# Performance work log

Measured on AMD Instinct MI355X. Metric: run time of the kernel, lower is better.

## Reference

```python
import jax, jax.numpy as jnp
import numpy as np

DIM = 768
HEADS = 12
HEAD_DIM = DIM // HEADS
MLP_DIM = 4 * DIM
EPS = 1e-5


def setup_inputs() -> dict:
    key = jax.random.key(0)
    ks = jax.random.split(key, 8)
    s = lambda fan_in: 1.0 / np.sqrt(fan_in)
    return {
        "x": jax.random.normal(ks[0], (2, 2048, DIM), dtype=jnp.float32),
        "ln1_w": jnp.ones((DIM,), jnp.float32),
        "ln1_b": jnp.zeros((DIM,), jnp.float32),
        # weights stored [in, out]
        "qkv_w": jax.random.normal(ks[1], (DIM, 3 * DIM), jnp.float32) * s(DIM),
        "qkv_b": jnp.zeros((3 * DIM,), jnp.float32),
        "proj_w": jax.random.normal(ks[2], (DIM, DIM), jnp.float32) * s(DIM),
        "proj_b": jnp.zeros((DIM,), jnp.float32),
        "ln2_w": jnp.ones((DIM,), jnp.float32),
        "ln2_b": jnp.zeros((DIM,), jnp.float32),
        "lin1_w": jax.random.normal(ks[3], (DIM, MLP_DIM), jnp.float32) * s(DIM),
        "lin1_b": jnp.zeros((MLP_DIM,), jnp.float32),
        "lin2_w": jax.random.normal(ks[4], (MLP_DIM, DIM), jnp.float32) * s(MLP_DIM),
        "lin2_b": jnp.zeros((DIM,), jnp.float32),
    }


def _layernorm(x, w, b):
    mu = jnp.mean(x, axis=-1, keepdims=True)
    var = jnp.mean(jnp.square(x - mu), axis=-1, keepdims=True)
    return (x - mu) * jax.lax.rsqrt(var + EPS) * w + b


def _attention(x, qkv_w, qkv_b, proj_w, proj_b):
    B, N, C = x.shape
    qkv = (x @ qkv_w + qkv_b).reshape(B, N, 3, HEADS, HEAD_DIM)
    q, k, v = qkv[:, :, 0], qkv[:, :, 1], qkv[:, :, 2]  # [B, N, H, Dh]
    scale = HEAD_DIM ** -0.5
    attn = jnp.einsum("bqhd,bkhd->bhqk", q, k) * scale  # full NxN scores
    attn = jax.nn.softmax(attn, axis=-1)
    out = jnp.einsum("bhqk,bkhd->bqhd", attn, v).reshape(B, N, C)
    return out @ proj_w + proj_b


def reference(x, ln1_w, ln1_b, qkv_w, qkv_b, proj_w, proj_b,
              ln2_w, ln2_b, lin1_w, lin1_b, lin2_w, lin2_b):
    x = x + _attention(_layernorm(x, ln1_w, ln1_b), qkv_w, qkv_b, proj_w, proj_b)
    h = _layernorm(x, ln2_w, ln2_b)
    h = jax.nn.gelu(h @ lin1_w + lin1_b, approximate=False) @ lin2_w + lin2_b
    return x + h
```

## Files before the change

### kernel.cpp

```cpp
#include <hip/hip_runtime.h>
#include <math.h>

#define DIM 768
#define NTOK 4096
#define SEQ 2048
#define HEADS 12
#define HD 64

using bf16x8 = __attribute__((ext_vector_type(8))) __bf16;
using f32x4  = __attribute__((ext_vector_type(4))) float;
typedef unsigned short u16;

__device__ inline u16 f2bf(float f) {
  union { float f; unsigned u; } v; v.f = f;
  unsigned r = v.u + 0x7fffu + ((v.u >> 16) & 1u);
  return (u16)(r >> 16);
}

__device__ inline void gl_lds16(const u16* g, u16* l) {
  __builtin_amdgcn_global_load_lds(
      (const __attribute__((address_space(1))) unsigned int*)g,
      (__attribute__((address_space(3))) unsigned int*)l, 16, 0, 0);
}

__global__ __launch_bounds__(256) void ln_kernel(const float* __restrict__ x,
                                                 const float* __restrict__ w,
                                                 const float* __restrict__ b,
                                                 u16* __restrict__ y) {
  int row = blockIdx.x;
  int t = threadIdx.x;
  const float* xr = x + (size_t)row * DIM;
  float v0 = xr[t], v1 = xr[t + 256], v2 = xr[t + 512];
  float s = v0 + v1 + v2;
  float q = v0 * v0 + v1 * v1 + v2 * v2;
  for (int o = 32; o > 0; o >>= 1) {
    s += __shfl_down(s, o, 64);
    q += __shfl_down(q, o, 64);
  }
  __shared__ float ws_[4], wq_[4], mb[2];
  int wid = t >> 6;
  if ((t & 63) == 0) { ws_[wid] = s; wq_[wid] = q; }
  __syncthreads();
  if (t == 0) {
    float S = ws_[0] + ws_[1] + ws_[2] + ws_[3];
    float Q = wq_[0] + wq_[1] + wq_[2] + wq_[3];
    float mean = S * (1.0f / DIM);
    float var = Q * (1.0f / DIM) - mean * mean;
    mb[0] = mean;
    mb[1] = rsqrtf(var + 1e-5f);
  }
  __syncthreads();
  float mean = mb[0], rstd = mb[1];
  u16* yr = y + (size_t)row * DIM;
  yr[t]       = f2bf((v0 - mean) * rstd * w[t]       + b[t]);
  yr[t + 256] = f2bf((v1 - mean) * rstd * w[t + 256] + b[t + 256]);
  yr[t + 512] = f2bf((v2 - mean) * rstd * w[t + 512] + b[t + 512]);
}

__global__ __launch_bounds__(256) void redln_kernel(
    const float* __restrict__ P0, const float* __restrict__ P1,
    const float* __restrict__ bias, const float* __restrict__ res,
    float* __restrict__ x2, const float* __restrict__ lnw,
    const float* __restrict__ lnb, u16* __restrict__ y) {
  int row = blockIdx.x;
  int t = threadIdx.x;
  size_t off = (size_t)row * DIM;
  float v[3];
#pragma unroll
  for (int k = 0; k < 3; ++k) {
    int c = t + k * 256;
    v[k] = P0[off + c] + P1[off + c] + bias[c] + res[off + c];
    x2[off + c] = v[k];
  }
  float s = v[0] + v[1] + v[2];
  float q = v[0] * v[0] + v[1] * v[1] + v[2] * v[2];
  for (int o = 32; o > 0; o >>= 1) {
    s += __shfl_down(s, o, 64);
    q += __shfl_down(q, o, 64);
  }
  __shared__ float ws_[4], wq_[4], mb[2];
  int wid = t >> 6;
  if ((t & 63) == 0) { ws_[wid] = s; wq_[wid] = q; }
  __syncthreads();
  if (t == 0) {
    float S = ws_[0] + ws_[1] + ws_[2] + ws_[3];
    float Q = wq_[0] + wq_[1] + wq_[2] + wq_[3];
    float mean = S * (1.0f / DIM);
    float var = Q * (1.0f / DIM) - mean * mean;
    mb[0] = mean;
    mb[1] = rsqrtf(var + 1e-5f);
  }
  __syncthreads();
  float mean = mb[0], rstd = mb[1];
#pragma unroll
  for (int k = 0; k < 3; ++k) {
    int c = t + k * 256;
    y[off + c] = f2bf((v[k] - mean) * rstd * lnw[c] + lnb[c]);
  }
}

__global__ __launch_bounds__(256) void wcvt_all(
    const float* __restrict__ W0, const float* __restrict__ W1,
    const float* __restrict__ W2, const float* __restrict__ W3,
    u16* __restrict__ T0, u16* __restrict__ T1,
    u16* __restrict__ T2, u16* __restrict__ T3) {
  int id = blockIdx.x;
  const float* W; u16* Wt; int K, N, local;
  if (id < 1728)      { W = W0; Wt = T0; K = 768;  N = 2304; local = id; }
  else if (id < 2304) { W = W1; Wt = T1; K = 768;  N = 768;  local = id - 1728; }
  else if (id < 4608) { W = W2; Wt = T2; K = 768;  N = 3072; local = id - 2304; }
  else                { W = W3; Wt = T3; K = 3072; N = 768;  local = id - 4608; }
  int ntiles = N / 32;
  int n0 = (local % ntiles) * 32, k0 = (local / ntiles) * 32;
  __shared__ float tile[32][33];
  int tid = threadIdx.x;
  int c = tid & 31, r8 = tid >> 5;
#pragma unroll
  for (int p = 0; p < 4; ++p) {
    int k = r8 + p * 8;
    tile[k][c] = W[(size_t)(k0 + k) * N + n0 + c];
  }
  __syncthreads();
#pragma unroll
  for (int p = 0; p < 4; ++p) {
    int n = r8 + p * 8;
    Wt[(size_t)(n0 + n) * K + k0 + c] = f2bf(tile[c][n]);
  }
}

__global__ __launch_bounds__(256) void vtr_kernel(const u16* __restrict__ qkvB,
                                                  u16* __restrict__ vT) {
  __shared__ u16 tile[32][33];
  int v0 = blockIdx.x * 32, j0 = blockIdx.y * 32, b = blockIdx.z;
  int tid = threadIdx.x;
  int c = tid & 31, r8 = tid >> 5;
#pragma unroll
  for (int p = 0; p < 4; ++p) {
    int r = r8 + p * 8;
    tile[r][c] = qkvB[((size_t)(b * SEQ + j0 + r)) * 2304 + 1536 + v0 + c];
  }
  __syncthreads();
#pragma unroll
  for (int p = 0; p < 4; ++p) {
    int r = r8 + p * 8;
    vT[((size_t)(b * 768 + v0 + r)) * SEQ + j0 + c] = tile[c][r];
  }
}

__global__ __launch_bounds__(256) void bgemm_kernel(
    const u16* __restrict__ A, const u16* __restrict__ Bt,
    const float* __restrict__ bias, u16* __restrict__ Cb,
    int M, int N, int K, int act) {
  __shared__ __align__(16) u16 Asl[128 * 32];
  __shared__ __align__(16) u16 Bsl[128 * 32];
  int tid = threadIdx.x;
  int lane = tid & 63, wave = tid >> 6;
  int wm = wave >> 1, wn = wave & 1;
  int bm = blockIdx.y * 128, bn = blockIdx.x * 128;
  int l15 = lane & 15, quad = lane >> 4;
  int sm = tid >> 2, kg = tid & 3;

  f32x4 acc[4][4] = {};
  const u16* Ap = A + (size_t)(bm + sm) * K + kg * 8;
  const u16* Bp = Bt + (size_t)(bn + sm) * K + kg * 8;
  u16* Al = &Asl[(wave * 16) * 32];
  u16* Bl = &Bsl[(wave * 16) * 32];

  for (int k0 = 0; k0 < K; k0 += 32) {
    gl_lds16(Ap + k0, Al);
    gl_lds16(Ap + (size_t)64 * K + k0, Al + 64 * 32);
    gl_lds16(Bp + k0, Bl);
    gl_lds16(Bp + (size_t)64 * K + k0, Bl + 64 * 32);
    __syncthreads();
    bf16x8 af[4], bfr[4];
#pragma unroll
    for (int i = 0; i < 4; ++i) {
      af[i]  = *(const bf16x8*)&Asl[(wm * 64 + i * 16 + l15) * 32 + quad * 8];
      bfr[i] = *(const bf16x8*)&Bsl[(wn * 64 + i * 16 + l15) * 32 + quad * 8];
    }
#pragma unroll
    for (int i = 0; i < 4; ++i)
#pragma unroll
      for (int j = 0; j < 4; ++j)
        acc[i][j] = __builtin_amdgcn_mfma_f32_16x16x32_bf16(af[i], bfr[j], acc[i][j], 0, 0, 0);
    __syncthreads();
  }

#pragma unroll
  for (int i = 0; i < 4; ++i) {
#pragma unroll
    for (int j = 0; j < 4; ++j) {
      int n = bn + wn * 64 + j * 16 + l15;
      float bv = bias[n];
#pragma unroll
      for (int r = 0; r < 4; ++r) {
        int m = bm + wm * 64 + i * 16 + quad * 4 + r;
        float val = acc[i][j][r] + bv;
        if (act) val = 0.5f * val * (1.0f + erff(val * 0.70710678118f));
        Cb[(size_t)m * N + n] = f2bf(val);
      }
    }
  }
}

__global__ __launch_bounds__(256) void bgemm_splitk(
    const u16* __restrict__ A, const u16* __restrict__ Bt,
    float* __restrict__ P0, float* __restrict__ P1,
    int M, int N, int K) {
  __shared__ __align__(16) u16 Asl[128 * 32];
  __shared__ __align__(16) u16 Bsl[64 * 32];
  int tid = threadIdx.x;
  int lane = tid & 63, wave = tid >> 6;
  int wm = wave >> 1, wn = wave & 1;
  int bm = blockIdx.y * 128, bn = blockIdx.x * 64;
  int l15 = lane & 15, quad = lane >> 4;
  int sm = tid >> 2, kg = tid & 3;
  int half = K >> 1;
  int kbeg = blockIdx.z * half;

  f32x4 acc[4][2] = {};
  const u16* Ap = A + (size_t)(bm + sm) * K + kbeg + kg * 8;
  const u16* Bp = Bt + (size_t)(bn + sm) * K + kbeg + kg * 8;
  u16* Al = &Asl[(wave * 16) * 32];
  u16* Bl = &Bsl[(wave * 16) * 32];

  for (int k0 = 0; k0 < half; k0 += 32) {
    gl_lds16(Ap + k0, Al);
    gl_lds16(Ap + (size_t)64 * K + k0, Al + 64 * 32);
    gl_lds16(Bp + k0, Bl);
    __syncthreads();
    bf16x8 af[4], bfr[2];
#pragma unroll
    for (int i = 0; i < 4; ++i)
      af[i] = *(const bf16x8*)&Asl[(wm * 64 + i * 16 + l15) * 32 + quad * 8];
#pragma unroll
    for (int j = 0; j < 2; ++j)
      bfr[j] = *(const bf16x8*)&Bsl[(wn * 32 + j * 16 + l15) * 32 + quad * 8];
#pragma unroll
    for (int i = 0; i < 4; ++i)
#pragma unroll
      for (int j = 0; j < 2; ++j)
        acc[i][j] = __builtin_amdgcn_mfma_f32_16x16x32_bf16(af[i], bfr[j], acc[i][j], 0, 0, 0);
    __syncthreads();
  }

  float* P = blockIdx.z ? P1 : P0;
#pragma unroll
  for (int i = 0; i < 4; ++i) {
#pragma unroll
    for (int j = 0; j < 2; ++j) {
      int n = bn + wn * 32 + j * 16 + l15;
#pragma unroll
      for (int r = 0; r < 4; ++r) {
        int m = bm + wm * 64 + i * 16 + quad * 4 + r;
        P[(size_t)m * N + n] = acc[i][j][r];
      }
    }
  }
}

__global__ __launch_bounds__(256) void red_kernel(
    const float* P0, const float* __restrict__ P1,
    const float* __restrict__ bias, const float* __restrict__ res,
    float* O, int Ncols) {
  int i = blockIdx.x * 256 + threadIdx.x;
  float4 a = ((const float4*)P0)[i];
  float4 b = ((const float4*)P1)[i];
  float4 r = ((const float4*)res)[i];
  int col = (i * 4) % Ncols;
  float4 bi = *(const float4*)&bias[col];
  float4 o;
  o.x = a.x + b.x + r.x + bi.x;
  o.y = a.y + b.y + r.y + bi.y;
  o.z = a.z + b.z + r.z + bi.z;
  o.w = a.w + b.w + r.w + bi.w;
  ((float4*)O)[i] = o;
}

#define AST 72
__global__ __launch_bounds__(256) void attn_kernel(const u16* __restrict__ qkv,
                                                   const u16* __restrict__ vT,
                                                   u16* __restrict__ out) {
  __shared__ u16 Qs[64 * AST];
  __shared__ u16 Ks[64 * AST];
  __shared__ u16 Vt[64 * AST];
  __shared__ u16 Ps[64 * AST];

  int tid = threadIdx.x;
  int lane = tid & 63, wave = tid >> 6;
  int l15 = lane & 15, quad = lane >> 4;
  int qt = blockIdx.x * 64;
  int h = blockIdx.y, b = blockIdx.z;
  size_t base = (size_t)b * SEQ;
  int ROW8 = tid >> 3, KG = tid & 7;
  int VROW = tid >> 2, VG = tid & 3;
  const u16* vbase = vT + ((size_t)(b * HEADS + h) * HD) * SEQ;

#pragma unroll
  for (int p = 0; p < 2; ++p) {
    int r = ROW8 + p * 32;
    uint4 v = *(const uint4*)(qkv + (base + qt + r) * 2304 + h * HD + KG * 8);
    *(uint4*)&Qs[r * AST + KG * 8] = v;
  }

  f32x4 o_acc[4] = {};
  float l_part[4] = {0.f, 0.f, 0.f, 0.f};
  int sw = l15 >> 2;

  for (int kt = 0; kt < SEQ; kt += 64) {
#pragma unroll
    for (int p = 0; p < 2; ++p) {
      int r = ROW8 + p * 32;
      uint4 kv = *(const uint4*)(qkv + (base + kt + r) * 2304 + 768 + h * HD + KG * 8);
      *(uint4*)&Ks[r * AST + KG * 8] = kv;
      int g = VG + p * 4;
      uint4 vv = *(const uint4*)(vbase + (size_t)VROW * SEQ + kt + g * 8);
      *(uint4*)&Vt[VROW * AST + g * 8] = vv;
    }
    __syncthreads();

    f32x4 s_acc[4] = {};
#pragma unroll
    for (int ks = 0; ks < 2; ++ks) {
      bf16x8 aq = *(const bf16x8*)&Qs[(wave * 16 + l15) * AST + ks * 32 + quad * 8];
#pragma unroll
      for (int jt = 0; jt < 4; ++jt) {
        bf16x8 bk = *(const bf16x8*)&Ks[(jt * 16 + l15) * AST + ks * 32 + quad * 8];
        s_acc[jt] = __builtin_amdgcn_mfma_f32_16x16x32_bf16(aq, bk, s_acc[jt], 0, 0, 0);
      }
    }

#pragma unroll
    for (int r = 0; r < 4; ++r) {
      float p0 = __expf(s_acc[0][r] * 0.125f);
      float p1 = __expf(s_acc[1][r] * 0.125f);
      float p2 = __expf(s_acc[2][r] * 0.125f);
      float p3 = __expf(s_acc[3][r] * 0.125f);
      l_part[r] += p0 + p1 + p2 + p3;
      int prow = (wave * 16 + quad * 4 + r) * AST;
      Ps[prow + ((0 ^ quad) * 16) + l15] = f2bf(p0);
      Ps[prow + ((1 ^ quad) * 16) + l15] = f2bf(p1);
      Ps[prow + ((2 ^ quad) * 16) + l15] = f2bf(p2);
      Ps[prow + ((3 ^ quad) * 16) + l15] = f2bf(p3);
    }
    __syncthreads();

#pragma unroll
    for (int ks = 0; ks < 2; ++ks) {
      int blk = ks * 2 + (quad >> 1);
      bf16x8 ap = *(const bf16x8*)&Ps[(wave * 16 + l15) * AST + ((blk ^ sw) * 16) + (quad & 1) * 8];
#pragma unroll
      for (int dt = 0; dt < 4; ++dt) {
        bf16x8 bv = *(const bf16x8*)&Vt[(dt * 16 + l15) * AST + ks * 32 + quad * 8];
        o_acc[dt] = __builtin_amdgcn_mfma_f32_16x16x32_bf16(ap, bv, o_acc[dt], 0, 0, 0);
      }
    }
    __syncthreads();
  }

#pragma unroll
  for (int r = 0; r < 4; ++r) {
    float l = l_part[r];
    for (int msk = 1; msk < 16; msk <<= 1) l += __shfl_xor(l, msk, 64);
    l_part[r] = 1.0f / l;
  }

#pragma unroll
  for (int r = 0; r < 4; ++r) {
    size_t trow = (base + qt + wave * 16 + quad * 4 + r) * DIM + h * HD;
#pragma unroll
    for (int dt = 0; dt < 4; ++dt)
      out[trow + dt * 16 + l15] = f2bf(o_acc[dt][r] * l_part[r]);
  }
}

extern "C" void kernel_launch(void* const* d_in, const int* in_sizes, int n_in,
                              void* d_out, int out_size, void* d_ws, size_t ws_size,
                              hipStream_t stream) {
  const float* x     = (const float*)d_in[0];
  const float* ln1w  = (const float*)d_in[1];
  const float* ln1b  = (const float*)d_in[2];
  const float* qkvw  = (const float*)d_in[3];
  const float* qkvbi = (const float*)d_in[4];
  const float* projw = (const float*)d_in[5];
  const float* projb = (const float*)d_in[6];
  const float* ln2w  = (const float*)d_in[7];
  const float* ln2b  = (const float*)d_in[8];
  const float* l1w   = (const float*)d_in[9];
  const float* l1b   = (const float*)d_in[10];
  const float* l2w   = (const float*)d_in[11];
  const float* l2b   = (const float*)d_in[12];
  float* out = (float*)d_out;

  char* w = (char*)d_ws;
  u16*   h     = (u16*)w;   w += (size_t)NTOK * DIM * 2;
  u16*   qkvB  = (u16*)w;
  u16*   mid   = (u16*)w;   w += (size_t)NTOK * 3072 * 2;
  u16*   attnb = (u16*)w;   w += (size_t)NTOK * DIM * 2;
  float* x2    = (float*)w; w += (size_t)NTOK * DIM * 4;
  u16*   vTb   = (u16*)w;   w += (size_t)NTOK * DIM * 2;
  u16*   qkvwt = (u16*)w;   w += (size_t)DIM * 2304 * 2;
  u16*   projwt= (u16*)w;   w += (size_t)DIM * DIM * 2;
  u16*   l1wt  = (u16*)w;   w += (size_t)DIM * 3072 * 2;
  u16*   l2wt  = (u16*)w;   w += (size_t)3072 * DIM * 2;
  float* Pbuf  = (float*)w; w += (size_t)NTOK * DIM * 4;

  wcvt_all<<<6912, 256, 0, stream>>>(qkvw, projw, l1w, l2w,
                                     qkvwt, projwt, l1wt, l2wt);

  ln_kernel<<<NTOK, 256, 0, stream>>>(x, ln1w, ln1b, h);
  bgemm_kernel<<<dim3(2304 / 128, NTOK / 128), 256, 0, stream>>>(
      h, qkvwt, qkvbi, qkvB, NTOK, 2304, DIM, 0);
  vtr_kernel<<<dim3(768 / 32, SEQ / 32, 2), 256, 0, stream>>>(qkvB, vTb);
  attn_kernel<<<dim3(SEQ / 64, HEADS, 2), 256, 0, stream>>>(qkvB, vTb, attnb);

  bgemm_splitk<<<dim3(DIM / 64, NTOK / 128, 2), 256, 0, stream>>>(
      attnb, projwt, x2, Pbuf, NTOK, DIM, DIM);
  redln_kernel<<<NTOK, 256, 0, stream>>>(x2, Pbuf, projb, x, x2, ln2w, ln2b, h);

  bgemm_kernel<<<dim3(3072 / 128, NTOK / 128), 256, 0, stream>>>(
      h, l1wt, l1b, mid, NTOK, 3072, DIM, 1);

  bgemm_splitk<<<dim3(DIM / 64, NTOK / 128, 2), 256, 0, stream>>>(
      mid, l2wt, out, Pbuf, NTOK, DIM, 3072);
  red_kernel<<<NTOK * DIM / 1024, 256, 0, stream>>>(out, Pbuf, l2b, x2, out, DIM);
}
```

Baseline: 321.8 us.

## Use tanh-form GELU, packed bf16 conversions, and hoist Q fragments in attention

Replaces the erf-based GELU in the GEMM epilogue with a tanh approximation written as a sigmoid using __expf. Swaps the manual float-to-bf16 rounding for the packed __float22bfloat162_rn conversion in the GEMM epilogue, the softmax P writes and the attention output. Q fragments are loaded into registers once before the key loop instead of reloaded from LDS on every tile, with an added barrier. The GELU approximation changes numerics slightly relative to the exact erf reference.

```diff
diff --git a/kernel.cpp b/kernel.cpp
--- a/kernel.cpp
+++ b/kernel.cpp
@@ -1,4 +1,5 @@
 #include <hip/hip_runtime.h>
+#include <hip/hip_bf16.h>
 #include <math.h>
 
 #define DIM 768
@@ -15,6 +16,18 @@
   union { float f; unsigned u; } v; v.f = f;
   unsigned r = v.u + 0x7fffu + ((v.u >> 16) & 1u);
   return (u16)(r >> 16);
+}
+
+__device__ inline void pk2bf(float a, float b, u16* o0, u16* o1) {
+  union { __hip_bfloat162 h; u16 u[2]; } cv;
+  cv.h = __float22bfloat162_rn(make_float2(a, b));
+  *o0 = cv.u[0];
+  *o1 = cv.u[1];
+}
+
+__device__ inline float gelu_t(float x) {
+  float z = x * (1.5957691216f + 0.0713548162f * x * x);
+  return x / (1.0f + __expf(-z));
 }
 
 __device__ inline void gl_lds16(const u16* g, u16* l) {
@@ -192,13 +205,20 @@
     for (int j = 0; j < 4; ++j) {
       int n = bn + wn * 64 + j * 16 + l15;
       float bv = bias[n];
+      float val[4];
 #pragma unroll
       for (int r = 0; r < 4; ++r) {
-        int m = bm + wm * 64 + i * 16 + quad * 4 + r;
-        float val = acc[i][j][r] + bv;
-        if (act) val = 0.5f * val * (1.0f + erff(val * 0.70710678118f));
-        Cb[(size_t)m * N + n] = f2bf(val);
+        float v = acc[i][j][r] + bv;
+        val[r] = act ? gelu_t(v) : v;
       }
+      u16 c0, c1, c2, c3;
+      pk2bf(val[0], val[1], &c0, &c1);
+      pk2bf(val[2], val[3], &c2, &c3);
+      size_t mbase = (size_t)(bm + wm * 64 + i * 16 + quad * 4) * N + n;
+      Cb[mbase]         = c0;
+      Cb[mbase + N]     = c1;
+      Cb[mbase + 2 * N] = c2;
+      Cb[mbase + 3 * N] = c3;
     }
   }
 }
@@ -302,6 +322,9 @@
     uint4 v = *(const uint4*)(qkv + (base + qt + r) * 2304 + h * HD + KG * 8);
     *(uint4*)&Qs[r * AST + KG * 8] = v;
   }
+  __syncthreads();
+  bf16x8 aq0 = *(const bf16x8*)&Qs[(wave * 16 + l15) * AST + 0 * 32 + quad * 8];
+  bf16x8 aq1 = *(const bf16x8*)&Qs[(wave * 16 + l15) * AST + 1 * 32 + quad * 8];
 
   f32x4 o_acc[4] = {};
   float l_part[4] = {0.f, 0.f, 0.f, 0.f};
@@ -321,13 +344,11 @@
 
     f32x4 s_acc[4] = {};
 #pragma unroll
-    for (int ks = 0; ks < 2; ++ks) {
-      bf16x8 aq = *(const bf16x8*)&Qs[(wave * 16 + l15) * AST + ks * 32 + quad * 8];
-#pragma unroll
-      for (int jt = 0; jt < 4; ++jt) {
-        bf16x8 bk = *(const bf16x8*)&Ks[(jt * 16 + l15) * AST + ks * 32 + quad * 8];
-        s_acc[jt] = __builtin_amdgcn_mfma_f32_16x16x32_bf16(aq, bk, s_acc[jt], 0, 0, 0);
-      }
+    for (int jt = 0; jt < 4; ++jt) {
+      bf16x8 bk0 = *(const bf16x8*)&Ks[(jt * 16 + l15) * AST + 0 * 32 + quad * 8];
+      s_acc[jt] = __builtin_amdgcn_mfma_f32_16x16x32_bf16(aq0, bk0, s_acc[jt], 0, 0, 0);
+      bf16x8 bk1 = *(const bf16x8*)&Ks[(jt * 16 + l15) * AST + 1 * 32 + quad * 8];
+      s_acc[jt] = __builtin_amdgcn_mfma_f32_16x16x32_bf16(aq1, bk1, s_acc[jt], 0, 0, 0);
     }
 
 #pragma unroll
@@ -337,11 +358,14 @@
       float p2 = __expf(s_acc[2][r] * 0.125f);
       float p3 = __expf(s_acc[3][r] * 0.125f);
       l_part[r] += p0 + p1 + p2 + p3;
+      u16 b0, b1, b2, b3;
+      pk2bf(p0, p1, &b0, &b1);
+      pk2bf(p2, p3, &b2, &b3);
       int prow = (wave * 16 + quad * 4 + r) * AST;
-      Ps[prow + ((0 ^ quad) * 16) + l15] = f2bf(p0);
-      Ps[prow + ((1 ^ quad) * 16) + l15] = f2bf(p1);
-      Ps[prow + ((2 ^ quad) * 16) + l15] = f2bf(p2);
-      Ps[prow + ((3 ^ quad) * 16) + l15] = f2bf(p3);
+      Ps[prow + ((0 ^ quad) * 16) + l15] = b0;
+      Ps[prow + ((1 ^ quad) * 16) + l15] = b1;
+      Ps[prow + ((2 ^ quad) * 16) + l15] = b2;
+      Ps[prow + ((3 ^ quad) * 16) + l15] = b3;
     }
     __syncthreads();
 
@@ -368,9 +392,13 @@
 #pragma unroll
   for (int r = 0; r < 4; ++r) {
     size_t trow = (base + qt + wave * 16 + quad * 4 + r) * DIM + h * HD;
-#pragma unroll
-    for (int dt = 0; dt < 4; ++dt)
-      out[trow + dt * 16 + l15] = f2bf(o_acc[dt][r] * l_part[r]);
+    u16 c0, c1, c2, c3;
+    pk2bf(o_acc[0][r] * l_part[r], o_acc[1][r] * l_part[r], &c0, &c1);
+    pk2bf(o_acc[2][r] * l_part[r], o_acc[3][r] * l_part[r], &c2, &c3);
+    out[trow + 0 * 16 + l15] = c0;
+    out[trow + 1 * 16 + l15] = c1;
+    out[trow + 2 * 16 + l15] = c2;
+    out[trow + 3 * 16 + l15] = c3;
   }
 }
 
```

Result: faster. 312.5 us (-2.9%).
